# Optimization experiments

Hardware: AMD Instinct MI355X
Metric: run time of the kernel (lower is better)

## Reference

```python
import jax, jax.numpy as jnp
import numpy as np

D_MODEL = 1024
N_HEADS = 16
D_HEAD = D_MODEL // N_HEADS
LN_EPS = 1e-5


def setup_inputs() -> dict:
    key = jax.random.key(0)
    ks = jax.random.split(key, 8)
    B, T = 4, 2048
    s = 1.0 / np.sqrt(D_MODEL)
    return {
        "encoder_seq": jax.random.normal(ks[0], (B, T, D_MODEL), jnp.float32),
        "decoder_seq": jax.random.normal(ks[1], (B, T, D_MODEL), jnp.float32),
        "Wq": jax.random.normal(ks[2], (D_MODEL, D_MODEL), jnp.float32) * s,
        "bq": jnp.zeros((D_MODEL,), jnp.float32),
        "Wk": jax.random.normal(ks[3], (D_MODEL, D_MODEL), jnp.float32) * s,
        "bk": jnp.zeros((D_MODEL,), jnp.float32),
        "Wv": jax.random.normal(ks[4], (D_MODEL, D_MODEL), jnp.float32) * s,
        "bv": jnp.zeros((D_MODEL,), jnp.float32),
        "ln_gamma": jnp.ones((D_MODEL,), jnp.float32),
        "ln_beta": jnp.zeros((D_MODEL,), jnp.float32),
    }


def layer_norm(x, gamma, beta):
    mu = jnp.mean(x, axis=-1, keepdims=True)
    var = jnp.mean(jnp.square(x - mu), axis=-1, keepdims=True)
    return (x - mu) * jax.lax.rsqrt(var + LN_EPS) * gamma + beta


def reference(encoder_seq, decoder_seq, Wq, bq, Wk, bk, Wv, bv, ln_gamma, ln_beta):
    B, T_dec, _ = decoder_seq.shape
    T_enc = encoder_seq.shape[1]
    # projections (torch Linear: x @ W^T + b)
    q = (decoder_seq @ Wq.T + bq).reshape(B, T_dec, N_HEADS, D_HEAD)
    k = (encoder_seq @ Wk.T + bk).reshape(B, T_enc, N_HEADS, D_HEAD)
    v = (encoder_seq @ Wv.T + bv).reshape(B, T_enc, N_HEADS, D_HEAD)
    scale = 1.0 / np.sqrt(D_HEAD)
    # softmax-free attention: scale*(Q K^T) V == scale * Q (K^T V); avoid [T_dec,T_enc]
    kv = jnp.einsum("bthd,bthe->bhde", k, v)          # [B,H,dh,dh]
    att = jnp.einsum("bqhd,bhde->bqhe", q, kv) * scale  # [B,T_dec,H,dh]
    att = att.reshape(B, T_dec, D_MODEL)
    # dropout is identity in eval mode; residual + LayerNorm
    return layer_norm(att + decoder_seq, ln_gamma, ln_beta)
```

## Files before the change

kernel.cpp:

```cpp
#include <hip/hip_runtime.h>
#include <hip/hip_bf16.h>
#include <stdint.h>
#include <stddef.h>

typedef __attribute__((ext_vector_type(8))) __bf16 bf16x8;
typedef __attribute__((ext_vector_type(4))) float f32x4;

#define DMODEL 1024
#define HEADS  16
#define BATCH  4
#define TSEQ   2048
#define MROWS  (BATCH * TSEQ)
#define NE     (MROWS * DMODEL)
#define NW     (DMODEL * DMODEL)

#define MiB (size_t)1048576
#define QB_OFF   ((size_t)0)
#define KB_OFF   (16 * MiB)
#define VB_OFF   (32 * MiB)
#define ENC_OFF  (48 * MiB)
#define DEC_OFF  (64 * MiB)
#define KVP_OFF  (64 * MiB)
#define WB_OFF   (80 * MiB)
#define KVT_OFF  (86 * MiB)

__global__ __launch_bounds__(256)
void conv_all(const float* __restrict__ enc, const float* __restrict__ dec,
              const float* __restrict__ Wq, const float* __restrict__ Wk,
              const float* __restrict__ Wv,
              __bf16* __restrict__ encB, __bf16* __restrict__ decB,
              __bf16* __restrict__ WB)
{
    const int i = (blockIdx.x * 256 + threadIdx.x) * 8;
    const float* src;
    __bf16* dst;
    int off;
    if (i < NE)            { src = enc; dst = encB; off = i; }
    else if (i < 2 * NE)   { src = dec; dst = decB; off = i - NE; }
    else {
        const int j = i - 2 * NE;
        const int sel = j >> 20;
        off = j & (NW - 1);
        src = (sel == 0) ? Wq : (sel == 1) ? Wk : Wv;
        dst = WB + (size_t)sel * NW;
    }
    f32x4 a = *(const f32x4*)(src + off);
    f32x4 b = *(const f32x4*)(src + off + 4);
    bf16x8 o;
#pragma unroll
    for (int j = 0; j < 4; ++j) { o[j] = (__bf16)a[j]; o[j + 4] = (__bf16)b[j]; }
    *(bf16x8*)(dst + off) = o;
}

__device__ __forceinline__ bf16x8 frag(const __bf16* reg, int rowl, int kh, int g4)
{
    const int slot = ((kh << 2) + g4) ^ (rowl & 7);
    return *(const bf16x8*)(reg + rowl * 64 + slot * 8);
}

__device__ __forceinline__ void stage_half256(const __bf16* gbase, int kt,
                                              __bf16* reg, int tid)
{
#pragma unroll
    for (int p = 0; p < 4; ++p) {
        const int c = tid + p * 256;
        const int row = c >> 3, slot = c & 7;
        const __bf16* src = gbase + (size_t)row * DMODEL + kt * 64
                            + ((slot ^ (row & 7)) << 3);
        __builtin_amdgcn_global_load_lds(
            (const __attribute__((address_space(1))) void*)src,
            (__attribute__((address_space(3))) void*)(reg + c * 8), 16, 0, 0);
    }
}

#define VMW(N)  asm volatile("s_waitcnt vmcnt(" #N ")" ::: "memory")

__global__ __launch_bounds__(256, 1)
void qkv_gemm(const __bf16* __restrict__ decB, const __bf16* __restrict__ encB,
              const __bf16* __restrict__ WB,
              const float* __restrict__ bq, const float* __restrict__ bk,
              const float* __restrict__ bv,
              __bf16* __restrict__ Qb, __bf16* __restrict__ Kb,
              __bf16* __restrict__ Vb)
{
    __shared__ __align__(16) __bf16 ldsA[3 * 8192];
    __shared__ __align__(16) __bf16 ldsB[3 * 16384];

    const int tid  = threadIdx.x;
    const int lane = tid & 63;
    const int wn   = tid >> 6;
    const int bh2  = wn >> 1;
    const int l4   = lane & 15;
    const int g4   = lane >> 4;

    const int bid  = blockIdx.x;
    const int slab = bid & 7;
    const int idx  = bid >> 3;
    const int r    = idx >> 3;
    const int sel  = r >> 2;
    const int bn   = r & 3;
    const int bm   = slab * 8 + (idx & 7);

    const __bf16* A    = (sel == 0) ? decB : encB;
    const __bf16* W    = WB + (size_t)sel * NW;
    const float*  bias = (sel == 0) ? bq : (sel == 1) ? bk : bv;
    __bf16*       C    = (sel == 0) ? Qb : (sel == 1) ? Kb : Vb;

    const __bf16* Ab = A + (size_t)(bm * 128) * DMODEL;
    const __bf16* Wb = W + (size_t)(bn * 256) * DMODEL;

    auto stage_tile = [&](int buf, int kt) {
        stage_half256(Ab,                        kt, ldsA + buf * 8192,          tid);
        stage_half256(Wb,                        kt, ldsB + buf * 16384,         tid);
        stage_half256(Wb + (size_t)128 * DMODEL, kt, ldsB + buf * 16384 + 8192,  tid);
    };

    f32x4 acc[8][4] = {};

    stage_tile(0, 0);
    stage_tile(1, 1);
    VMW(12);
    __builtin_amdgcn_sched_barrier(0);
    __builtin_amdgcn_s_barrier();

    int rd = 0, st = 2;
#pragma unroll 1
    for (int t = 0; t < 16; ++t) {
        const __bf16* bA = ldsA + rd * 8192;
        const __bf16* bB = ldsB + rd * 16384 + bh2 * 8192;

        bf16x8 af[8][2], bf[4][2];
#pragma unroll
        for (int mf = 0; mf < 8; ++mf)
#pragma unroll
            for (int kh = 0; kh < 2; ++kh)
                af[mf][kh] = frag(bA, mf * 16 + l4, kh, g4);
#pragma unroll
        for (int nf = 0; nf < 4; ++nf)
#pragma unroll
            for (int kh = 0; kh < 2; ++kh)
                bf[nf][kh] = frag(bB, (wn & 1) * 64 + nf * 16 + l4, kh, g4);

        if (t < 14) stage_tile(st, t + 2);

#pragma unroll
        for (int mf = 0; mf < 8; ++mf)
#pragma unroll
            for (int nf = 0; nf < 4; ++nf)
#pragma unroll
                for (int kh = 0; kh < 2; ++kh)
                    acc[mf][nf] = __builtin_amdgcn_mfma_f32_16x16x32_bf16(
                        af[mf][kh], bf[nf][kh], acc[mf][nf], 0, 0, 0);

        if (t < 14)      { VMW(12); }
        else if (t == 14){ VMW(0);  }
        __builtin_amdgcn_sched_barrier(0);
        __builtin_amdgcn_s_barrier();

        rd = (rd == 2) ? 0 : rd + 1;
        st = (st == 2) ? 0 : st + 1;
    }

#pragma unroll
    for (int mf = 0; mf < 8; ++mf)
#pragma unroll
        for (int nf = 0; nf < 4; ++nf) {
            const int gm0 = bm * 128 + mf * 16 + g4 * 4;
            const int gn  = bn * 256 + wn * 64 + nf * 16 + l4;
            const float bv2 = bias[gn];
#pragma unroll
            for (int j = 0; j < 4; ++j)
                C[(size_t)(gm0 + j) * DMODEL + gn] =
                    (__bf16)(acc[mf][nf][j] + bv2);
        }
}

__global__ __launch_bounds__(256)
void kv_mm(const __bf16* __restrict__ Kb, const __bf16* __restrict__ Vb,
           float* __restrict__ kvp)
{
    __shared__ __align__(16) float Ks[128][64];
    __shared__ __align__(16) float Vs[128][64];

    const int tid = threadIdx.x;
    const int bh  = blockIdx.x;
    const int ch  = blockIdx.y;
    const int b   = bh >> 4, h = bh & 15;
    const int w   = tid >> 6, lane = tid & 63;
    const int dg  = (lane >> 3) * 8;
    const int eg  = (lane & 7) * 8;
    const size_t base = (size_t)b * TSEQ + (size_t)ch * 512;

    f32x4 acc[8][2] = {};

    for (int ss = 0; ss < 4; ++ss) {
        __syncthreads();
#pragma unroll
        for (int i = 0; i < 4; ++i) {
            const int e = i * 2048 + tid * 8;
            const int t = e >> 6, d = e & 63;
            bf16x8 k8 = *(const bf16x8*)&Kb[(base + ss * 128 + t) * DMODEL + h * 64 + d];
            bf16x8 v8 = *(const bf16x8*)&Vb[(base + ss * 128 + t) * DMODEL + h * 64 + d];
            f32x4 kf0, kf1, vf0, vf1;
#pragma unroll
            for (int j = 0; j < 4; ++j) {
                kf0[j] = (float)k8[j]; kf1[j] = (float)k8[j + 4];
                vf0[j] = (float)v8[j]; vf1[j] = (float)v8[j + 4];
            }
            *(f32x4*)&Ks[t][d]     = kf0;
            *(f32x4*)&Ks[t][d + 4] = kf1;
            *(f32x4*)&Vs[t][d]     = vf0;
            *(f32x4*)&Vs[t][d + 4] = vf1;
        }
        __syncthreads();

#pragma unroll 4
        for (int tt = 0; tt < 32; ++tt) {
            const int t = w * 32 + tt;
            f32x4 kd0 = *(const f32x4*)&Ks[t][dg];
            f32x4 kd1 = *(const f32x4*)&Ks[t][dg + 4];
            f32x4 ve0 = *(const f32x4*)&Vs[t][eg];
            f32x4 ve1 = *(const f32x4*)&Vs[t][eg + 4];
#pragma unroll
            for (int rr = 0; rr < 8; ++rr) {
                const float kd = (rr < 4) ? kd0[rr] : kd1[rr - 4];
                acc[rr][0] += ve0 * kd;
                acc[rr][1] += ve1 * kd;
            }
        }
    }

    float* o = kvp + ((size_t)(ch * 4 + w) * 64 + bh) * 4096 + (size_t)dg * 64 + eg;
#pragma unroll
    for (int rr = 0; rr < 8; ++rr) {
        *(f32x4*)(o + rr * 64)     = acc[rr][0];
        *(f32x4*)(o + rr * 64 + 4) = acc[rr][1];
    }
}

__global__ __launch_bounds__(256)
void kv_reduce(const float* __restrict__ kvp, __bf16* __restrict__ kvT)
{
    const int idx = blockIdx.x * 256 + threadIdx.x;
    const int bh  = idx >> 12;
    const int rem = idx & 4095;
    const int d = rem >> 6, e = rem & 63;
    float s = 0.f;
#pragma unroll
    for (int c = 0; c < 16; ++c) s += kvp[((size_t)c * 64 + bh) * 4096 + rem];
    kvT[(size_t)bh * 4096 + e * 64 + d] = (__bf16)(s * 0.125f);
}

__global__ __launch_bounds__(256)
void att_ln(const __bf16* __restrict__ Q, const __bf16* __restrict__ kvT,
            const float* __restrict__ dec, const float* __restrict__ gamma,
            const float* __restrict__ beta, float* __restrict__ out)
{
    __shared__ __align__(16) __bf16 att_s[32][1032];

    const int tid  = threadIdx.x;
    const int lane = tid & 63;
    const int w    = tid >> 6;
    const int l4   = lane & 15, g4 = lane >> 4;
    const int t0   = blockIdx.x * 32;
    const int b    = t0 >> 11;

#pragma unroll
    for (int i = 0; i < 4; ++i) {
        const int h = w * 4 + i;
        f32x4 acc[2][4] = {};
#pragma unroll
        for (int kk = 0; kk < 2; ++kk) {
            bf16x8 a0 = *(const bf16x8*)&Q[(size_t)(t0 + l4) * DMODEL + h * 64 + kk * 32 + g4 * 8];
            bf16x8 a1 = *(const bf16x8*)&Q[(size_t)(t0 + 16 + l4) * DMODEL + h * 64 + kk * 32 + g4 * 8];
#pragma unroll
            for (int n = 0; n < 4; ++n) {
                bf16x8 bb = *(const bf16x8*)&kvT[(size_t)(b * 16 + h) * 4096 + (n * 16 + l4) * 64 + kk * 32 + g4 * 8];
                acc[0][n] = __builtin_amdgcn_mfma_f32_16x16x32_bf16(a0, bb, acc[0][n], 0, 0, 0);
                acc[1][n] = __builtin_amdgcn_mfma_f32_16x16x32_bf16(a1, bb, acc[1][n], 0, 0, 0);
            }
        }
#pragma unroll
        for (int m = 0; m < 2; ++m)
#pragma unroll
            for (int n = 0; n < 4; ++n)
#pragma unroll
                for (int j = 0; j < 4; ++j)
                    att_s[m * 16 + g4 * 4 + j][h * 64 + n * 16 + l4] = (__bf16)acc[m][n][j];
    }
    __syncthreads();

    const int rr = tid >> 3, seg = tid & 7;
    const size_t grow = (size_t)t0 + rr;
    float sum = 0.f, ss2 = 0.f;
#pragma unroll
    for (int i = 0; i < 16; ++i) {
        const int c0 = seg * 8 + i * 64;
        bf16x8 av = *(const bf16x8*)&att_s[rr][c0];
        f32x4 d0 = *(const f32x4*)&dec[grow * DMODEL + c0];
        f32x4 d1 = *(const f32x4*)&dec[grow * DMODEL + c0 + 4];
        bf16x8 xs;
#pragma unroll
        for (int j = 0; j < 4; ++j) {
            const float x0 = (float)av[j] + d0[j];
            const float x1 = (float)av[j + 4] + d1[j];
            sum += x0 + x1; ss2 += x0 * x0 + x1 * x1;
            xs[j] = (__bf16)x0; xs[j + 4] = (__bf16)x1;
        }
        *(bf16x8*)&att_s[rr][c0] = xs;
    }
    sum += __shfl_xor(sum, 1); ss2 += __shfl_xor(ss2, 1);
    sum += __shfl_xor(sum, 2); ss2 += __shfl_xor(ss2, 2);
    sum += __shfl_xor(sum, 4); ss2 += __shfl_xor(ss2, 4);
    const float mu   = sum * (1.f / 1024.f);
    const float var  = ss2 * (1.f / 1024.f) - mu * mu;
    const float rstd = rsqrtf(var + 1e-5f);

#pragma unroll
    for (int i = 0; i < 16; ++i) {
        const int c0 = seg * 8 + i * 64;
        bf16x8 xv = *(const bf16x8*)&att_s[rr][c0];
        f32x4 g0 = *(const f32x4*)&gamma[c0];
        f32x4 g1 = *(const f32x4*)&gamma[c0 + 4];
        f32x4 b0 = *(const f32x4*)&beta[c0];
        f32x4 b1 = *(const f32x4*)&beta[c0 + 4];
        f32x4 y0, y1;
#pragma unroll
        for (int j = 0; j < 4; ++j) {
            y0[j] = ((float)xv[j]     - mu) * rstd * g0[j] + b0[j];
            y1[j] = ((float)xv[j + 4] - mu) * rstd * g1[j] + b1[j];
        }
        *(f32x4*)&out[grow * DMODEL + c0]     = y0;
        *(f32x4*)&out[grow * DMODEL + c0 + 4] = y1;
    }
}

extern "C" void kernel_launch(void* const* d_in, const int* in_sizes, int n_in,
                              void* d_out, int out_size, void* d_ws, size_t ws_size,
                              hipStream_t stream)
{
    const float* enc   = (const float*)d_in[0];
    const float* dec   = (const float*)d_in[1];
    const float* Wq    = (const float*)d_in[2];
    const float* bq    = (const float*)d_in[3];
    const float* Wk    = (const float*)d_in[4];
    const float* bk    = (const float*)d_in[5];
    const float* Wv    = (const float*)d_in[6];
    const float* bv    = (const float*)d_in[7];
    const float* gamma = (const float*)d_in[8];
    const float* beta  = (const float*)d_in[9];

    char* ws = (char*)d_ws;
    __bf16* Qb   = (__bf16*)(ws + QB_OFF);
    __bf16* Kb   = (__bf16*)(ws + KB_OFF);
    __bf16* Vb   = (__bf16*)(ws + VB_OFF);
    __bf16* encB = (__bf16*)(ws + ENC_OFF);
    __bf16* decB = (__bf16*)(ws + DEC_OFF);
    float*  kvp  = (float*) (ws + KVP_OFF);
    __bf16* WB   = (__bf16*)(ws + WB_OFF);
    __bf16* kvT  = (__bf16*)(ws + KVT_OFF);

    conv_all<<<9728, 256, 0, stream>>>(enc, dec, Wq, Wk, Wv, encB, decB, WB);
    qkv_gemm<<<768, 256, 0, stream>>>(decB, encB, WB, bq, bk, bv, Qb, Kb, Vb);
    kv_mm<<<dim3(64, 4), 256, 0, stream>>>(Kb, Vb, kvp);
    kv_reduce<<<1024, 256, 0, stream>>>(kvp, kvT);
    att_ln<<<256, 256, 0, stream>>>(Qb, kvT, dec, gamma, beta, (float*)d_out);
}
```

Before: 132.3 us.

## Fuse activation fp32-to-bf16 conversion into QKV GEMM A-tile staging

The separate conversion pass over encoder and decoder activations is dropped; the QKV GEMM now reads fp32 activations from global memory into registers, converts them, and writes bf16 into LDS, while weights are still pre-converted by a smaller kernel. The GEMM moves to 512 threads in a 2x4 wave grid with double buffering in place of triple buffering, register prefetch of the A tile, and raised MFMA priority. This avoids writing and rereading 32 MiB of bf16 activations. The cost is twice the global read bytes for A inside the GEMM and a shallower pipeline with more barriers per iteration.

```diff
diff --git a/kernel.cpp b/kernel.cpp
--- a/kernel.cpp
+++ b/kernel.cpp
@@ -18,38 +18,24 @@
 #define QB_OFF   ((size_t)0)
 #define KB_OFF   (16 * MiB)
 #define VB_OFF   (32 * MiB)
-#define ENC_OFF  (48 * MiB)
-#define DEC_OFF  (64 * MiB)
-#define KVP_OFF  (64 * MiB)
-#define WB_OFF   (80 * MiB)
-#define KVT_OFF  (86 * MiB)
+#define KVP_OFF  (48 * MiB)
+#define WB_OFF   (64 * MiB)
+#define KVT_OFF  (70 * MiB)
 
 __global__ __launch_bounds__(256)
-void conv_all(const float* __restrict__ enc, const float* __restrict__ dec,
-              const float* __restrict__ Wq, const float* __restrict__ Wk,
-              const float* __restrict__ Wv,
-              __bf16* __restrict__ encB, __bf16* __restrict__ decB,
-              __bf16* __restrict__ WB)
-{
-    const int i = (blockIdx.x * 256 + threadIdx.x) * 8;
-    const float* src;
-    __bf16* dst;
-    int off;
-    if (i < NE)            { src = enc; dst = encB; off = i; }
-    else if (i < 2 * NE)   { src = dec; dst = decB; off = i - NE; }
-    else {
-        const int j = i - 2 * NE;
-        const int sel = j >> 20;
-        off = j & (NW - 1);
-        src = (sel == 0) ? Wq : (sel == 1) ? Wk : Wv;
-        dst = WB + (size_t)sel * NW;
-    }
-    f32x4 a = *(const f32x4*)(src + off);
-    f32x4 b = *(const f32x4*)(src + off + 4);
+void conv_w(const float* __restrict__ Wq, const float* __restrict__ Wk,
+            const float* __restrict__ Wv, __bf16* __restrict__ WB)
+{
+    const int bid = blockIdx.x;
+    const int sel = bid >> 9, blk = bid & 511;
+    const float* src = (sel == 0) ? Wq : (sel == 1) ? Wk : Wv;
+    const int i = blk * 2048 + threadIdx.x * 8;
+    f32x4 a = *(const f32x4*)(src + i);
+    f32x4 b = *(const f32x4*)(src + i + 4);
     bf16x8 o;
 #pragma unroll
     for (int j = 0; j < 4; ++j) { o[j] = (__bf16)a[j]; o[j + 4] = (__bf16)b[j]; }
-    *(bf16x8*)(dst + off) = o;
+    *(bf16x8*)&WB[(size_t)sel * NW + i] = o;
 }
 
 __device__ __forceinline__ bf16x8 frag(const __bf16* reg, int rowl, int kh, int g4)
@@ -58,12 +44,12 @@
     return *(const bf16x8*)(reg + rowl * 64 + slot * 8);
 }
 
-__device__ __forceinline__ void stage_half256(const __bf16* gbase, int kt,
-                                              __bf16* reg, int tid)
-{
-#pragma unroll
-    for (int p = 0; p < 4; ++p) {
-        const int c = tid + p * 256;
+__device__ __forceinline__ void stage_halfB(const __bf16* gbase, int kt,
+                                            __bf16* reg, int tid)
+{
+#pragma unroll
+    for (int p = 0; p < 2; ++p) {
+        const int c = tid + p * 512;
         const int row = c >> 3, slot = c & 7;
         const __bf16* src = gbase + (size_t)row * DMODEL + kt * 64
                             + ((slot ^ (row & 7)) << 3);
@@ -74,21 +60,24 @@
 }
 
 #define VMW(N)  asm volatile("s_waitcnt vmcnt(" #N ")" ::: "memory")
-
-__global__ __launch_bounds__(256, 1)
-void qkv_gemm(const __bf16* __restrict__ decB, const __bf16* __restrict__ encB,
+#define LGKM0() asm volatile("s_waitcnt lgkmcnt(0)" ::: "memory")
+
+__global__ __launch_bounds__(512, 2)
+void qkv_gemm(const float* __restrict__ dec, const float* __restrict__ enc,
               const __bf16* __restrict__ WB,
               const float* __restrict__ bq, const float* __restrict__ bk,
               const float* __restrict__ bv,
               __bf16* __restrict__ Qb, __bf16* __restrict__ Kb,
               __bf16* __restrict__ Vb)
 {
-    __shared__ __align__(16) __bf16 ldsA[3 * 8192];
-    __shared__ __align__(16) __bf16 ldsB[3 * 16384];
+    __shared__ __align__(16) __bf16 ldsA[2 * 8192];
+    __shared__ __align__(16) __bf16 ldsB[2 * 16384];
 
     const int tid  = threadIdx.x;
     const int lane = tid & 63;
-    const int wn   = tid >> 6;
+    const int wv   = tid >> 6;
+    const int wm   = wv >> 2;
+    const int wn   = wv & 3;
     const int bh2  = wn >> 1;
     const int l4   = lane & 15;
     const int g4   = lane >> 4;
@@ -101,71 +90,98 @@
     const int bn   = r & 3;
     const int bm   = slab * 8 + (idx & 7);
 
-    const __bf16* A    = (sel == 0) ? decB : encB;
-    const __bf16* W    = WB + (size_t)sel * NW;
+    const float*  Afp  = ((sel == 0) ? dec : enc) + (size_t)(bm * 128) * DMODEL;
+    const __bf16* Wb   = WB + (size_t)sel * NW + (size_t)(bn * 256) * DMODEL;
     const float*  bias = (sel == 0) ? bq : (sel == 1) ? bk : bv;
     __bf16*       C    = (sel == 0) ? Qb : (sel == 1) ? Kb : Vb;
 
-    const __bf16* Ab = A + (size_t)(bm * 128) * DMODEL;
-    const __bf16* Wb = W + (size_t)(bn * 256) * DMODEL;
-
-    auto stage_tile = [&](int buf, int kt) {
-        stage_half256(Ab,                        kt, ldsA + buf * 8192,          tid);
-        stage_half256(Wb,                        kt, ldsB + buf * 16384,         tid);
-        stage_half256(Wb + (size_t)128 * DMODEL, kt, ldsB + buf * 16384 + 8192,  tid);
+    const int c0 = tid, c1 = tid + 512;
+    const int rA0 = c0 >> 3, sA0 = ((c0 & 7) ^ (rA0 & 7)) << 3;
+    const int rA1 = c1 >> 3, sA1 = ((c1 & 7) ^ (rA1 & 7)) << 3;
+
+    f32x4 alr[4];
+    auto loadA = [&](int kt, f32x4* ar) {
+        const float* p0 = Afp + (size_t)rA0 * DMODEL + kt * 64 + sA0;
+        const float* p1 = Afp + (size_t)rA1 * DMODEL + kt * 64 + sA1;
+        ar[0] = *(const f32x4*)p0; ar[1] = *(const f32x4*)(p0 + 4);
+        ar[2] = *(const f32x4*)p1; ar[3] = *(const f32x4*)(p1 + 4);
     };
-
-    f32x4 acc[8][4] = {};
-
-    stage_tile(0, 0);
-    stage_tile(1, 1);
-    VMW(12);
+    auto writeA = [&](int par, const f32x4* ar) {
+        bf16x8 o0, o1;
+#pragma unroll
+        for (int j = 0; j < 4; ++j) {
+            o0[j] = (__bf16)ar[0][j]; o0[j + 4] = (__bf16)ar[1][j];
+            o1[j] = (__bf16)ar[2][j]; o1[j + 4] = (__bf16)ar[3][j];
+        }
+        *(bf16x8*)(ldsA + par * 8192 + c0 * 8) = o0;
+        *(bf16x8*)(ldsA + par * 8192 + c1 * 8) = o1;
+    };
+    auto stageB = [&](int par, int kt) {
+        stage_halfB(Wb,                        kt, ldsB + par * 16384,        tid);
+        stage_halfB(Wb + (size_t)128 * DMODEL, kt, ldsB + par * 16384 + 8192, tid);
+    };
+
+    f32x4 acc[4][4] = {};
+
+    { f32x4 t0r[4]; loadA(0, t0r); VMW(0); writeA(0, t0r); }
+    { f32x4 t1r[4]; loadA(1, t1r); VMW(0); writeA(1, t1r); }
+    stageB(0, 0);
+    stageB(1, 1);
+    loadA(2, alr);
+    VMW(8);
+    LGKM0();
     __builtin_amdgcn_sched_barrier(0);
     __builtin_amdgcn_s_barrier();
 
-    int rd = 0, st = 2;
 #pragma unroll 1
     for (int t = 0; t < 16; ++t) {
-        const __bf16* bA = ldsA + rd * 8192;
-        const __bf16* bB = ldsB + rd * 16384 + bh2 * 8192;
-
-        bf16x8 af[8][2], bf[4][2];
-#pragma unroll
-        for (int mf = 0; mf < 8; ++mf)
+        const int par = t & 1;
+        const __bf16* bA = ldsA + par * 8192;
+        const __bf16* bB = ldsB + par * 16384 + bh2 * 8192;
+
+        bf16x8 af[4][2], bf[4][2];
+#pragma unroll
+        for (int mf = 0; mf < 4; ++mf)
 #pragma unroll
             for (int kh = 0; kh < 2; ++kh)
-                af[mf][kh] = frag(bA, mf * 16 + l4, kh, g4);
+                af[mf][kh] = frag(bA, wm * 64 + mf * 16 + l4, kh, g4);
 #pragma unroll
         for (int nf = 0; nf < 4; ++nf)
 #pragma unroll
             for (int kh = 0; kh < 2; ++kh)
                 bf[nf][kh] = frag(bB, (wn & 1) * 64 + nf * 16 + l4, kh, g4);
 
-        if (t < 14) stage_tile(st, t + 2);
-
-#pragma unroll
-        for (int mf = 0; mf < 8; ++mf)
+        LGKM0();
+        __builtin_amdgcn_sched_barrier(0);
+        __builtin_amdgcn_s_barrier();
+
+        if (t <= 14) { VMW(0); }
+        if (t <= 13) {
+            writeA(par, alr);
+            stageB(par, t + 2);
+        }
+        if (t <= 12) loadA(t + 3, alr);
+
+        __builtin_amdgcn_sched_barrier(0);
+        __builtin_amdgcn_s_setprio(1);
+#pragma unroll
+        for (int mf = 0; mf < 4; ++mf)
 #pragma unroll
             for (int nf = 0; nf < 4; ++nf)
 #pragma unroll
                 for (int kh = 0; kh < 2; ++kh)
                     acc[mf][nf] = __builtin_amdgcn_mfma_f32_16x16x32_bf16(
                         af[mf][kh], bf[nf][kh], acc[mf][nf], 0, 0, 0);
-
-        if (t < 14)      { VMW(12); }
-        else if (t == 14){ VMW(0);  }
+        __builtin_amdgcn_s_setprio(0);
         __builtin_amdgcn_sched_barrier(0);
         __builtin_amdgcn_s_barrier();
-
-        rd = (rd == 2) ? 0 : rd + 1;
-        st = (st == 2) ? 0 : st + 1;
-    }
-
-#pragma unroll
-    for (int mf = 0; mf < 8; ++mf)
+    }
+
+#pragma unroll
+    for (int mf = 0; mf < 4; ++mf)
 #pragma unroll
         for (int nf = 0; nf < 4; ++nf) {
-            const int gm0 = bm * 128 + mf * 16 + g4 * 4;
+            const int gm0 = bm * 128 + wm * 64 + mf * 16 + g4 * 4;
             const int gn  = bn * 256 + wn * 64 + nf * 16 + l4;
             const float bv2 = bias[gn];
 #pragma unroll
@@ -351,17 +367,15 @@
     const float* beta  = (const float*)d_in[9];
 
     char* ws = (char*)d_ws;
-    __bf16* Qb   = (__bf16*)(ws + QB_OFF);
-    __bf16* Kb   = (__bf16*)(ws + KB_OFF);
-    __bf16* Vb   = (__bf16*)(ws + VB_OFF);
-    __bf16* encB = (__bf16*)(ws + ENC_OFF);
-    __bf16* decB = (__bf16*)(ws + DEC_OFF);
-    float*  kvp  = (float*) (ws + KVP_OFF);
-    __bf16* WB   = (__bf16*)(ws + WB_OFF);
-    __bf16* kvT  = (__bf16*)(ws + KVT_OFF);
-
-    conv_all<<<9728, 256, 0, stream>>>(enc, dec, Wq, Wk, Wv, encB, decB, WB);
-    qkv_gemm<<<768, 256, 0, stream>>>(decB, encB, WB, bq, bk, bv, Qb, Kb, Vb);
+    __bf16* Qb  = (__bf16*)(ws + QB_OFF);
+    __bf16* Kb  = (__bf16*)(ws + KB_OFF);
+    __bf16* Vb  = (__bf16*)(ws + VB_OFF);
+    float*  kvp = (float*) (ws + KVP_OFF);
+    __bf16* WB  = (__bf16*)(ws + WB_OFF);
+    __bf16* kvT = (__bf16*)(ws + KVT_OFF);
+
+    conv_w<<<1536, 256, 0, stream>>>(Wq, Wk, Wv, WB);
+    qkv_gemm<<<768, 512, 0, stream>>>(dec, enc, WB, bq, bk, bv, Qb, Kb, Vb);
     kv_mm<<<dim3(64, 4), 256, 0, stream>>>(Kb, Vb, kvp);
     kv_reduce<<<1024, 256, 0, stream>>>(kvp, kvT);
     att_ln<<<256, 256, 0, stream>>>(Qb, kvT, dec, gamma, beta, (float*)d_out);
```

After: 129.3 us. 2.3% less time.

## Restructure QKV GEMM to 512 threads, BK=32 double-buffered LDS, higher occupancy

Applied to the files above, without the earlier changes.

The QKV projection GEMM moves from 4 waves per block with a 64-wide K tile and triple-buffered LDS to 8 waves (2x4 warp grid) with a 32-wide K tile and double buffering. Per-wave accumulators shrink from 8x4 to 4x4 fragments and LDS use falls, so several blocks can share a CU (launch bounds 512,4) and global loads are hidden by occupancy rather than deep prefetch. MFMA sections are raised in wave priority with s_setprio, and a new swizzle keeps LDS reads conflict-free for the narrower rows. The cost is twice as many K iterations, each with two barriers and an lgkmcnt wait, so there is more synchronization overhead per unit of math.

```diff
diff --git a/kernel.cpp b/kernel.cpp
--- a/kernel.cpp
+++ b/kernel.cpp
@@ -52,30 +52,29 @@
     *(bf16x8*)(dst + off) = o;
 }
 
-__device__ __forceinline__ bf16x8 frag(const __bf16* reg, int rowl, int kh, int g4)
-{
-    const int slot = ((kh << 2) + g4) ^ (rowl & 7);
-    return *(const bf16x8*)(reg + rowl * 64 + slot * 8);
-}
-
-__device__ __forceinline__ void stage_half256(const __bf16* gbase, int kt,
-                                              __bf16* reg, int tid)
-{
-#pragma unroll
-    for (int p = 0; p < 4; ++p) {
-        const int c = tid + p * 256;
-        const int row = c >> 3, slot = c & 7;
-        const __bf16* src = gbase + (size_t)row * DMODEL + kt * 64
-                            + ((slot ^ (row & 7)) << 3);
-        __builtin_amdgcn_global_load_lds(
-            (const __attribute__((address_space(1))) void*)src,
-            (__attribute__((address_space(3))) void*)(reg + c * 8), 16, 0, 0);
-    }
+__device__ __forceinline__ int swz4(int row) { return (row & 3) ^ ((row >> 2) & 3); }
+
+__device__ __forceinline__ bf16x8 frag32(const __bf16* reg, int rowl, int g4)
+{
+    const int slot = g4 ^ swz4(rowl);
+    return *(const bf16x8*)(reg + rowl * 32 + slot * 8);
+}
+
+__device__ __forceinline__ void stage_half32(const __bf16* gbase, int kt,
+                                             __bf16* reg, int tid)
+{
+    const int row = tid >> 2, slot = tid & 3;
+    const __bf16* src = gbase + (size_t)row * DMODEL + kt * 32
+                        + ((slot ^ swz4(row)) << 3);
+    __builtin_amdgcn_global_load_lds(
+        (const __attribute__((address_space(1))) void*)src,
+        (__attribute__((address_space(3))) void*)(reg + tid * 8), 16, 0, 0);
 }
 
 #define VMW(N)  asm volatile("s_waitcnt vmcnt(" #N ")" ::: "memory")
-
-__global__ __launch_bounds__(256, 1)
+#define LGKM0() asm volatile("s_waitcnt lgkmcnt(0)" ::: "memory")
+
+__global__ __launch_bounds__(512, 4)
 void qkv_gemm(const __bf16* __restrict__ decB, const __bf16* __restrict__ encB,
               const __bf16* __restrict__ WB,
               const float* __restrict__ bq, const float* __restrict__ bk,
@@ -83,12 +82,14 @@
               __bf16* __restrict__ Qb, __bf16* __restrict__ Kb,
               __bf16* __restrict__ Vb)
 {
-    __shared__ __align__(16) __bf16 ldsA[3 * 8192];
-    __shared__ __align__(16) __bf16 ldsB[3 * 16384];
+    __shared__ __align__(16) __bf16 ldsA[2 * 4096];
+    __shared__ __align__(16) __bf16 ldsB[2 * 8192];
 
     const int tid  = threadIdx.x;
     const int lane = tid & 63;
-    const int wn   = tid >> 6;
+    const int wv   = tid >> 6;
+    const int wm   = wv >> 2;
+    const int wn   = wv & 3;
     const int bh2  = wn >> 1;
     const int l4   = lane & 15;
     const int g4   = lane >> 4;
@@ -102,70 +103,67 @@
     const int bm   = slab * 8 + (idx & 7);
 
     const __bf16* A    = (sel == 0) ? decB : encB;
-    const __bf16* W    = WB + (size_t)sel * NW;
+    const __bf16* Wb   = WB + (size_t)sel * NW + (size_t)(bn * 256) * DMODEL;
     const float*  bias = (sel == 0) ? bq : (sel == 1) ? bk : bv;
     __bf16*       C    = (sel == 0) ? Qb : (sel == 1) ? Kb : Vb;
 
     const __bf16* Ab = A + (size_t)(bm * 128) * DMODEL;
-    const __bf16* Wb = W + (size_t)(bn * 256) * DMODEL;
-
-    auto stage_tile = [&](int buf, int kt) {
-        stage_half256(Ab,                        kt, ldsA + buf * 8192,          tid);
-        stage_half256(Wb,                        kt, ldsB + buf * 16384,         tid);
-        stage_half256(Wb + (size_t)128 * DMODEL, kt, ldsB + buf * 16384 + 8192,  tid);
+
+    auto stage_tile = [&](int par, int kt) {
+        stage_half32(Ab,                        kt, ldsA + par * 4096,        tid);
+        stage_half32(Wb,                        kt, ldsB + par * 8192,        tid);
+        stage_half32(Wb + (size_t)128 * DMODEL, kt, ldsB + par * 8192 + 4096, tid);
     };
 
-    f32x4 acc[8][4] = {};
+    f32x4 acc[4][4] = {};
 
     stage_tile(0, 0);
     stage_tile(1, 1);
-    VMW(12);
+    VMW(3);
     __builtin_amdgcn_sched_barrier(0);
     __builtin_amdgcn_s_barrier();
 
-    int rd = 0, st = 2;
 #pragma unroll 1
-    for (int t = 0; t < 16; ++t) {
-        const __bf16* bA = ldsA + rd * 8192;
-        const __bf16* bB = ldsB + rd * 16384 + bh2 * 8192;
-
-        bf16x8 af[8][2], bf[4][2];
-#pragma unroll
-        for (int mf = 0; mf < 8; ++mf)
-#pragma unroll
-            for (int kh = 0; kh < 2; ++kh)
-                af[mf][kh] = frag(bA, mf * 16 + l4, kh, g4);
+    for (int t = 0; t < 32; ++t) {
+        const int par = t & 1;
+        const __bf16* bA = ldsA + par * 4096;
+        const __bf16* bB = ldsB + par * 8192 + bh2 * 4096;
+
+        bf16x8 af[4], bf[4];
+#pragma unroll
+        for (int mf = 0; mf < 4; ++mf)
+            af[mf] = frag32(bA, wm * 64 + mf * 16 + l4, g4);
 #pragma unroll
         for (int nf = 0; nf < 4; ++nf)
-#pragma unroll
-            for (int kh = 0; kh < 2; ++kh)
-                bf[nf][kh] = frag(bB, (wn & 1) * 64 + nf * 16 + l4, kh, g4);
-
-        if (t < 14) stage_tile(st, t + 2);
-
-#pragma unroll
-        for (int mf = 0; mf < 8; ++mf)
-#pragma unroll
-            for (int nf = 0; nf < 4; ++nf)
-#pragma unroll
-                for (int kh = 0; kh < 2; ++kh)
-                    acc[mf][nf] = __builtin_amdgcn_mfma_f32_16x16x32_bf16(
-                        af[mf][kh], bf[nf][kh], acc[mf][nf], 0, 0, 0);
-
-        if (t < 14)      { VMW(12); }
-        else if (t == 14){ VMW(0);  }
+            bf[nf] = frag32(bB, (wn & 1) * 64 + nf * 16 + l4, g4);
+
+        LGKM0();
         __builtin_amdgcn_sched_barrier(0);
         __builtin_amdgcn_s_barrier();
 
-        rd = (rd == 2) ? 0 : rd + 1;
-        st = (st == 2) ? 0 : st + 1;
-    }
-
-#pragma unroll
-    for (int mf = 0; mf < 8; ++mf)
+        if (t < 30) stage_tile(par, t + 2);
+
+        __builtin_amdgcn_sched_barrier(0);
+        __builtin_amdgcn_s_setprio(1);
+#pragma unroll
+        for (int mf = 0; mf < 4; ++mf)
+#pragma unroll
+            for (int nf = 0; nf < 4; ++nf)
+                acc[mf][nf] = __builtin_amdgcn_mfma_f32_16x16x32_bf16(
+                    af[mf], bf[nf], acc[mf][nf], 0, 0, 0);
+        __builtin_amdgcn_s_setprio(0);
+
+        if (t < 30)       { VMW(3); }
+        else if (t == 30) { VMW(0); }
+        __builtin_amdgcn_sched_barrier(0);
+        __builtin_amdgcn_s_barrier();
+    }
+
+#pragma unroll
+    for (int mf = 0; mf < 4; ++mf)
 #pragma unroll
         for (int nf = 0; nf < 4; ++nf) {
-            const int gm0 = bm * 128 + mf * 16 + g4 * 4;
+            const int gm0 = bm * 128 + wm * 64 + mf * 16 + g4 * 4;
             const int gn  = bn * 256 + wn * 64 + nf * 16 + l4;
             const float bv2 = bias[gn];
 #pragma unroll
@@ -361,7 +359,7 @@
     __bf16* kvT  = (__bf16*)(ws + KVT_OFF);
 
     conv_all<<<9728, 256, 0, stream>>>(enc, dec, Wq, Wk, Wv, encB, decB, WB);
-    qkv_gemm<<<768, 256, 0, stream>>>(decB, encB, WB, bq, bk, bv, Qb, Kb, Vb);
+    qkv_gemm<<<768, 512, 0, stream>>>(decB, encB, WB, bq, bk, bv, Qb, Kb, Vb);
     kv_mm<<<dim3(64, 4), 256, 0, stream>>>(Kb, Vb, kvp);
     kv_reduce<<<1024, 256, 0, stream>>>(kvp, kvT);
     att_ln<<<256, 256, 0, stream>>>(Qb, kvT, dec, gamma, beta, (float*)d_out);
```

Result: slower. 135.1 us (+2.2%).
